# Performance work log

Measured on AMD Instinct MI355X. Metric: run time of the kernel, lower is better.

The kernel has to match this reference:

```python
import jax, jax.numpy as jnp
import numpy as np

WS = 8        # window_size
NH = 8        # num_heads
LN_EPS = 1e-5

# static relative-position index table [WS*WS, WS*WS], values in [0, (2*WS-1)**2)
def _rel_index(ws):
    coords = np.arange(ws)
    grid = np.stack(np.meshgrid(coords, coords, indexing='ij')).reshape(2, -1)  # [2, W2]
    rel = grid[:, :, None] - grid[:, None, :]            # [2, W2, W2]
    rel = rel.transpose(1, 2, 0).copy()                   # [W2, W2, 2]
    rel[..., 0] += ws - 1
    rel[..., 1] += ws - 1
    rel[..., 0] *= 2 * ws - 1
    return rel.sum(-1)                                    # [W2, W2]

REL_IDX = jnp.asarray(_rel_index(WS))


def _ln(x):
    # LayerNorm without affine params (elementwise_affine=False)
    mu = jnp.mean(x, axis=-1, keepdims=True)
    var = jnp.var(x, axis=-1, keepdims=True)
    return (x - mu) * jax.lax.rsqrt(var + LN_EPS)


def setup_inputs() -> dict:
    key = jax.random.key(0)
    ks = jax.random.split(key, 16)
    B, Hg, Wg, C = 8, 64, 64, 256
    L = Hg * Wg
    s = 0.02
    inp = {
        'x': jax.random.normal(ks[0], (B, L, C), jnp.float32),
        't_embed': jax.random.normal(ks[1], (B, C), jnp.float32),
        'H': Hg,
        'W': Wg,
        'adaln1_w': s * jax.random.normal(ks[2], (C, 2 * C), jnp.float32),
        'adaln1_b': jnp.zeros((2 * C,), jnp.float32),
        'adaln2_w': s * jax.random.normal(ks[3], (C, 2 * C), jnp.float32),
        'adaln2_b': jnp.zeros((2 * C,), jnp.float32),
        'bias_table': s * jax.random.normal(ks[4], ((2 * WS - 1) ** 2, NH), jnp.float32),
        'q_w': s * jax.random.normal(ks[5], (C, C), jnp.float32),
        'q_b': jnp.zeros((C,), jnp.float32),
        'k_w': s * jax.random.normal(ks[6], (C, C), jnp.float32),
        'k_b': jnp.zeros((C,), jnp.float32),
        'v_w': s * jax.random.normal(ks[7], (C, C), jnp.float32),
        'v_b': jnp.zeros((C,), jnp.float32),
        'o_w': s * jax.random.normal(ks[8], (C, C), jnp.float32),
        'o_b': jnp.zeros((C,), jnp.float32),
        'ffn1_w': s * jax.random.normal(ks[9], (C, 4 * C), jnp.float32),
        'ffn1_b': jnp.zeros((4 * C,), jnp.float32),
        'ffn2_w': s * jax.random.normal(ks[10], (4 * C, C), jnp.float32),
        'ffn2_b': jnp.zeros((C,), jnp.float32),
    }
    return inp


def reference(x, t_embed, H, W, adaln1_w, adaln1_b, adaln2_w, adaln2_b,
              bias_table, q_w, q_b, k_w, k_b, v_w, v_b, o_w, o_b,
              ffn1_w, ffn1_b, ffn2_w, ffn2_b):
    B, L, C = x.shape
    d = C // NH
    W2 = WS * WS
    sh = WS // 2  # cyclic shift (shifted=True)

    # --- AdaLN1 ---
    ss = t_embed @ adaln1_w + adaln1_b              # [B, 2C]
    scale, shift = jnp.split(ss, 2, axis=-1)
    xn = _ln(x) * (1.0 + scale[:, None, :]) + shift[:, None, :]

    # --- shifted window partition ---
    xg = xn.reshape(B, H, W, C)
    xg = jnp.roll(xg, (-sh, -sh), axis=(1, 2))
    xw = xg.reshape(B, H // WS, WS, W // WS, WS, C).transpose(0, 1, 3, 2, 4, 5)
    xw = xw.reshape(-1, W2, C)                       # [nwB, W2, C]
    nwB = xw.shape[0]

    # --- window attention with relative position bias ---
    q = (xw @ q_w + q_b).reshape(nwB, W2, NH, d).transpose(0, 2, 1, 3)
    k = (xw @ k_w + k_b).reshape(nwB, W2, NH, d).transpose(0, 2, 1, 3)
    v = (xw @ v_w + v_b).reshape(nwB, W2, NH, d).transpose(0, 2, 1, 3)
    logits = jnp.einsum('whqd,whkd->whqk', q, k) * (d ** -0.5)
    bias = bias_table[REL_IDX.reshape(-1)].reshape(W2, W2, NH).transpose(2, 0, 1)
    logits = logits + bias[None].astype(logits.dtype)
    attn = jax.nn.softmax(logits, axis=-1)
    out = jnp.einsum('whqk,whkd->whqd', attn, v).transpose(0, 2, 1, 3).reshape(nwB, W2, C)
    out = out @ o_w + o_b

    # --- window reverse + unshift ---
    xm = out.reshape(B, H // WS, W // WS, WS, WS, C).transpose(0, 1, 3, 2, 4, 5)
    xm = xm.reshape(B, H, W, C)
    xm = jnp.roll(xm, (sh, sh), axis=(1, 2))
    x = x + xm.reshape(B, L, C)

    # --- AdaLN2 + FFN (GELU exact, matching torch nn.GELU) ---
    ss2 = t_embed @ adaln2_w + adaln2_b
    sc2, sh2 = jnp.split(ss2, 2, axis=-1)
    xn2 = _ln(x) * (1.0 + sc2[:, None, :]) + sh2[:, None, :]
    h = jax.nn.gelu(xn2 @ ffn1_w + ffn1_b, approximate=False)
    x = x + (h @ ffn2_w + ffn2_b)
    return x
```

## Files before the change

kernel.cpp:

```cpp
#include <hip/hip_runtime.h>
#include <math.h>

#define WS_ 8
#define NH_ 8
#define C_ 256
#define B_ 8
#define M_ 32768
#define SH_ 4
#define LN_EPS 1e-5f
#define SL_ 8388608

typedef __attribute__((ext_vector_type(8))) short bf16x8;
typedef __attribute__((ext_vector_type(4))) float f32x4;

__device__ inline float b2f(unsigned short u) {
    union { unsigned int i; float f; } c; c.i = ((unsigned int)u) << 16; return c.f;
}
__device__ inline unsigned short f2b(float f) {
    union { unsigned int i; float f; } c; c.f = f;
    unsigned int u = c.i;
    return (unsigned short)((u + 0x7FFFu + ((u >> 16) & 1u)) >> 16);
}
__device__ inline float gelu_f(float x) {
    float t = 1.59576912160573f * (x + 0.044715f * x * x * x);
    return x / (1.f + __expf(-t));
}

__global__ void prep_k(const float* __restrict__ qw, const float* __restrict__ kw,
                       const float* __restrict__ vw, const float* __restrict__ ow,
                       const float* __restrict__ f1w, const float* __restrict__ f2w,
                       const float* __restrict__ qb, const float* __restrict__ kb,
                       const float* __restrict__ vb, const float* __restrict__ bt,
                       const float* __restrict__ te,
                       const float* __restrict__ a1w, const float* __restrict__ a1b,
                       const float* __restrict__ a2w, const float* __restrict__ a2b,
                       unsigned short* __restrict__ qkvT, unsigned short* __restrict__ oT,
                       unsigned short* __restrict__ f1T, unsigned short* __restrict__ f2T,
                       float* __restrict__ qkvB, float* __restrict__ bias_full,
                       float* __restrict__ ss1, float* __restrict__ ss2) {
    int t = blockIdx.x * 256 + threadIdx.x;
    if (t < 196608) {
        int n = t >> 8, k = t & 255;
        const float* w = n < 256 ? qw : (n < 512 ? kw : vw);
        qkvT[t] = f2b(w[k * 256 + (n & 255)]);
    } else if (t < 262144) {
        int i = t - 196608; int n = i >> 8, k = i & 255;
        oT[i] = f2b(ow[k * 256 + n]);
    } else if (t < 524288) {
        int i = t - 262144; int n = i >> 8, k = i & 255;
        f1T[i] = f2b(f1w[k * 1024 + n]);
    } else if (t < 786432) {
        int i = t - 524288; int n = i >> 10, k = i & 1023;
        f2T[i] = f2b(f2w[k * 256 + n]);
    } else if (t < 787200) {
        int i = t - 786432;
        qkvB[i] = i < 256 ? qb[i] : (i < 512 ? kb[i - 256] : vb[i - 512]);
    } else if (t < 819968) {
        int i = t - 787200;
        int head = i >> 12, qk = i & 4095;
        int q = qk >> 6, k = qk & 63;
        int qh = q >> 3, qw2 = q & 7, kh = k >> 3, kw2 = k & 7;
        bias_full[i] = bt[((qh - kh + 7) * 15 + (qw2 - kw2 + 7)) * 8 + head];
    } else if (t < 828160) {
        int i = t - 819968;
        int which = i >> 12;
        int rem = i & 4095;
        int b = rem >> 9, col = rem & 511;
        const float* w = which ? a2w : a1w;
        const float* bb = which ? a2b : a1b;
        const float* tr = te + b * C_;
        float acc = bb[col];
        for (int k = 0; k < C_; ++k) acc += tr[k] * w[k * 512 + col];
        (which ? ss2 : ss1)[b * 512 + col] = acc;
    }
}

__global__ __launch_bounds__(256) void ln_win_k(const float* __restrict__ x,
                                                const float* __restrict__ ss,
                                                unsigned short* __restrict__ xw) {
    int t = blockIdx.x * 4 + (threadIdx.x >> 6);
    int lane = threadIdx.x & 63;
    int b = t >> 12, rem = t & 4095;
    int hg = rem >> 6, wg = rem & 63;
    int hs = (hg + SH_) & 63, wsrc = (wg + SH_) & 63;
    size_t src = ((size_t)b << 12) + (hs << 6) + wsrc;
    float4 v = *(const float4*)&x[src * C_ + lane * 4];
    float s = v.x + v.y + v.z + v.w;
    float s2 = v.x * v.x + v.y * v.y + v.z * v.z + v.w * v.w;
#pragma unroll
    for (int m = 1; m < 64; m <<= 1) { s += __shfl_xor(s, m); s2 += __shfl_xor(s2, m); }
    float mu = s * (1.f / 256.f);
    float rstd = rsqrtf(s2 * (1.f / 256.f) - mu * mu + LN_EPS);
    float4 sc = *(const float4*)&ss[b * 512 + lane * 4];
    float4 sh = *(const float4*)&ss[b * 512 + 256 + lane * 4];
    int win = (b << 6) + ((hg >> 3) << 3) + (wg >> 3);
    int pos = ((hg & 7) << 3) + (wg & 7);
    ushort4 pk;
    pk.x = f2b((v.x - mu) * rstd * (1.f + sc.x) + sh.x);
    pk.y = f2b((v.y - mu) * rstd * (1.f + sc.y) + sh.y);
    pk.z = f2b((v.z - mu) * rstd * (1.f + sc.z) + sh.z);
    pk.w = f2b((v.w - mu) * rstd * (1.f + sc.w) + sh.w);
    *(ushort4*)(xw + (size_t)(win * 64 + pos) * C_ + lane * 4) = pk;
}

template <int KDIM, int MODE, int NT>
__global__ __launch_bounds__(512, 2) void gemmv_k(
    const unsigned short* __restrict__ A, const unsigned short* __restrict__ Bt,
    const float* __restrict__ bias, const float* __restrict__ res,
    void* __restrict__ Cout, const float* __restrict__ ss2,
    unsigned short* __restrict__ xn2out, int Nout) {
    constexpr int NCH = KDIM / 256;
    constexpr int NBUF = (NCH > 1) ? 2 : 1;
    __shared__ __align__(16) unsigned short As[NBUF][128 * 256];

    const int blk = blockIdx.x;
    const int xcd = blk & 7;
    const int idx = blk >> 3;
    const int mt = xcd + ((idx / NT) << 3);
    const int nt = idx % NT;
    const int bm = mt * 128, bn = nt * 256;
    const int tid = threadIdx.x;
    const int w = tid >> 6, lane = tid & 63;
    const int quad = lane >> 4, l16 = lane & 15;
    const int wrow = (w >> 2) * 64;
    const int wcol = (w & 3) * 64;
    const int srow16 = tid >> 5;
    const int sc = tid & 31;

    f32x4 acc[4][4] = {};

    auto stageA = [&](int buf, int kc) {
#pragma unroll
        for (int p = 0; p < 8; ++p) {
            int row = p * 16 + srow16;
            int g = sc ^ (row & 7);
            const unsigned short* ga = A + (size_t)(bm + row) * KDIM + kc * 256 + g * 8;
            unsigned short* la = &As[buf][row * 256 + sc * 8];
            __builtin_amdgcn_global_load_lds(
                (const __attribute__((address_space(1))) void*)ga,
                (__attribute__((address_space(3))) void*)la, 16, 0, 0);
        }
    };

    auto computeC = [&](int buf, int kc) {
        const unsigned short* bp = Bt + (size_t)(bn + wcol + l16) * KDIM + kc * 256 + quad * 8;
#pragma unroll
        for (int k8 = 0; k8 < 8; ++k8) {
            bf16x8 bfr[4], af[4];
#pragma unroll
            for (int j = 0; j < 4; ++j)
                bfr[j] = *(const bf16x8*)(bp + (size_t)j * 16 * KDIM + k8 * 32);
#pragma unroll
            for (int i = 0; i < 4; ++i) {
                int row = wrow + i * 16 + l16;
                int cidx = (k8 * 4 + quad) ^ (row & 7);
                af[i] = *(const bf16x8*)&As[buf][row * 256 + cidx * 8];
            }
            __builtin_amdgcn_s_setprio(1);
#pragma unroll
            for (int i = 0; i < 4; ++i)
#pragma unroll
                for (int j = 0; j < 4; ++j)
                    acc[i][j] = __builtin_amdgcn_mfma_f32_16x16x32_bf16(
                        bfr[j], af[i], acc[i][j], 0, 0, 0);
            __builtin_amdgcn_s_setprio(0);
        }
    };

    stageA(0, 0);
    asm volatile("s_waitcnt vmcnt(0)" ::: "memory");
    __builtin_amdgcn_s_barrier();
    if constexpr (NCH == 1) {
        computeC(0, 0);
    } else {
#pragma unroll
        for (int c = 0; c < NCH; ++c) {
            if (c + 1 < NCH) stageA((c + 1) & 1, c + 1);
            computeC(c & 1, c);
            if (c + 1 < NCH) {
                asm volatile("s_waitcnt vmcnt(0)" ::: "memory");
                __builtin_amdgcn_s_barrier();
            }
        }
    }

    if (MODE == 1) {
        float ps[4], ps2[4];
#pragma unroll
        for (int i = 0; i < 4; ++i) {
            const int row = bm + wrow + i * 16 + l16;
            int win = row >> 6, pos = row & 63;
            int b = win >> 6, wh = (win >> 3) & 7, ww = win & 7;
            int hg = (wh << 3) + (pos >> 3), wg = (ww << 3) + (pos & 7);
            int hd = (hg + SH_) & 63, wd = (wg + SH_) & 63;
            size_t rowbase = (((size_t)b << 12) + (hd << 6) + wd) * C_;
            float s = 0.f, s2 = 0.f;
#pragma unroll
            for (int j = 0; j < 4; ++j) {
                const int col = bn + wcol + j * 16 + quad * 4;
                float4 bv = *(const float4*)&bias[col];
                float4 rv = *(const float4*)&res[rowbase + col];
                float4 ov = {acc[i][j][0] + bv.x + rv.x, acc[i][j][1] + bv.y + rv.y,
                             acc[i][j][2] + bv.z + rv.z, acc[i][j][3] + bv.w + rv.w};
                *(float4*)&((float*)Cout)[rowbase + col] = ov;
                acc[i][j][0] = ov.x; acc[i][j][1] = ov.y;
                acc[i][j][2] = ov.z; acc[i][j][3] = ov.w;
                s += ov.x + ov.y + ov.z + ov.w;
                s2 += ov.x * ov.x + ov.y * ov.y + ov.z * ov.z + ov.w * ov.w;
            }
            ps[i] = s; ps2[i] = s2;
        }
#pragma unroll
        for (int i = 0; i < 4; ++i) {
            ps[i] += __shfl_xor(ps[i], 16);  ps[i] += __shfl_xor(ps[i], 32);
            ps2[i] += __shfl_xor(ps2[i], 16); ps2[i] += __shfl_xor(ps2[i], 32);
        }
        float* sred = (float*)&As[0][0];
        asm volatile("s_waitcnt lgkmcnt(0)" ::: "memory");
        __builtin_amdgcn_s_barrier();
        if (quad == 0) {
#pragma unroll
            for (int i = 0; i < 4; ++i) {
                int r = i * 16 + l16;
                sred[(w * 64 + r) * 2 + 0] = ps[i];
                sred[(w * 64 + r) * 2 + 1] = ps2[i];
            }
        }
        __builtin_amdgcn_s_barrier();
#pragma unroll
        for (int i = 0; i < 4; ++i) {
            int r = i * 16 + l16;
            float s = 0.f, s2 = 0.f;
#pragma unroll
            for (int cw = 0; cw < 4; ++cw) {
                s  += sred[(((w >> 2) * 4 + cw) * 64 + r) * 2 + 0];
                s2 += sred[(((w >> 2) * 4 + cw) * 64 + r) * 2 + 1];
            }
            float mu = s * (1.f / 256.f);
            float rstd = rsqrtf(s2 * (1.f / 256.f) - mu * mu + LN_EPS);
            const int row = bm + wrow + i * 16 + l16;
            int win = row >> 6, pos = row & 63;
            int b = win >> 6, wh = (win >> 3) & 7, ww = win & 7;
            int hg = (wh << 3) + (pos >> 3), wg = (ww << 3) + (pos & 7);
            int hd = (hg + SH_) & 63, wd = (wg + SH_) & 63;
            size_t rowbase = (((size_t)b << 12) + (hd << 6) + wd) * C_;
#pragma unroll
            for (int j = 0; j < 4; ++j) {
                const int col = bn + wcol + j * 16 + quad * 4;
                float4 scv = *(const float4*)&ss2[b * 512 + col];
                float4 shv = *(const float4*)&ss2[b * 512 + 256 + col];
                ushort4 pk;
                pk.x = f2b((acc[i][j][0] - mu) * rstd * (1.f + scv.x) + shv.x);
                pk.y = f2b((acc[i][j][1] - mu) * rstd * (1.f + scv.y) + shv.y);
                pk.z = f2b((acc[i][j][2] - mu) * rstd * (1.f + scv.z) + shv.z);
                pk.w = f2b((acc[i][j][3] - mu) * rstd * (1.f + scv.w) + shv.w);
                *(ushort4*)(xn2out + rowbase + col) = pk;
            }
        }
        return;
    }

#pragma unroll
    for (int i = 0; i < 4; ++i) {
        const int row = bm + wrow + i * 16 + l16;
        size_t rowbase = 0;
        if (MODE == 0) {
            int win = row >> 6, pos = row & 63;
            rowbase = (size_t)win * 16384 + pos * 32;
        } else {
            rowbase = (size_t)row * Nout;
        }
#pragma unroll
        for (int j = 0; j < 4; ++j) {
            const int col = bn + wcol + j * 16 + quad * 4;
            float4 bv = *(const float4*)&bias[col];
            float v0 = acc[i][j][0] + bv.x, v1 = acc[i][j][1] + bv.y;
            float v2 = acc[i][j][2] + bv.z, v3 = acc[i][j][3] + bv.w;
            if (MODE == 0) {
                int which = col >> 8, head = (col >> 5) & 7, dc = col & 31;
                ushort4 pk = {f2b(v0), f2b(v1), f2b(v2), f2b(v3)};
                *(ushort4*)((unsigned short*)Cout + (size_t)which * SL_ + rowbase +
                            head * 2048 + dc) = pk;
            } else if (MODE == 2) {
                ushort4 pk = {f2b(gelu_f(v0)), f2b(gelu_f(v1)),
                              f2b(gelu_f(v2)), f2b(gelu_f(v3))};
                *(ushort4*)((unsigned short*)Cout + rowbase + col) = pk;
            } else {
                float4 rv = *(const float4*)&res[rowbase + col];
                float4 ov = {v0 + rv.x, v1 + rv.y, v2 + rv.z, v3 + rv.w};
                *(float4*)&((float*)Cout)[rowbase + col] = ov;
            }
        }
    }
}

__global__ __launch_bounds__(256) void attn_mfma_k(
    const unsigned short* __restrict__ qkv, const float* __restrict__ bias_full,
    unsigned short* __restrict__ attn_out) {
    __shared__ __align__(16) unsigned short Pb[4][64 * 66];
    __shared__ __align__(16) unsigned short Vt[4][32 * 66];
    const int w = threadIdx.x >> 6, lane = threadIdx.x & 63;
    const int wh = blockIdx.x * 4 + w;
    const int win = wh >> 3, head = wh & 7;
    const int quad = lane >> 4, l16 = lane & 15;

    const unsigned short* qp = qkv + (size_t)win * 16384 + head * 2048;
    const unsigned short* kp = qp + SL_;
    const unsigned short* vp = qp + 2 * (size_t)SL_;

    {
        const uint4* v4 = (const uint4*)(vp + lane * 32);
        unsigned short* dst = &Vt[w][0];
#pragma unroll
        for (int c = 0; c < 4; ++c) {
            uint4 u = v4[c];
            unsigned int uu[4] = {u.x, u.y, u.z, u.w};
#pragma unroll
            for (int p = 0; p < 4; ++p) {
                int d0 = c * 8 + p * 2;
                dst[d0 * 66 + lane] = (unsigned short)(uu[p] & 0xffff);
                dst[(d0 + 1) * 66 + lane] = (unsigned short)(uu[p] >> 16);
            }
        }
    }

    bf16x8 qf[4], kf[4];
#pragma unroll
    for (int i = 0; i < 4; ++i) {
        qf[i] = *(const bf16x8*)(qp + (i * 16 + l16) * 32 + quad * 8);
        kf[i] = *(const bf16x8*)(kp + (i * 16 + l16) * 32 + quad * 8);
    }

    f32x4 s[4][4] = {};
#pragma unroll
    for (int i = 0; i < 4; ++i)
#pragma unroll
        for (int j = 0; j < 4; ++j)
            s[i][j] = __builtin_amdgcn_mfma_f32_16x16x32_bf16(qf[i], kf[j], s[i][j], 0, 0, 0);

    const float scale = 0.17677669529663687f;
    const float* bf = bias_full + head * 4096;
    float rs[4][4];
#pragma unroll
    for (int i = 0; i < 4; ++i) {
#pragma unroll
        for (int r = 0; r < 4; ++r) {
            int row = i * 16 + quad * 4 + r;
            float acc = 0.f;
#pragma unroll
            for (int j = 0; j < 4; ++j) {
                float e = __expf(s[i][j][r] * scale + bf[row * 64 + j * 16 + l16]);
                s[i][j][r] = e;
                acc += e;
            }
#pragma unroll
            for (int msk = 1; msk < 16; msk <<= 1) acc += __shfl_xor(acc, msk);
            rs[i][r] = 1.f / acc;
        }
    }

#pragma unroll
    for (int i = 0; i < 4; ++i)
#pragma unroll
        for (int j = 0; j < 4; ++j)
#pragma unroll
            for (int r = 0; r < 4; ++r)
                Pb[w][(i * 16 + quad * 4 + r) * 66 + j * 16 + l16] = f2b(s[i][j][r]);

    __syncthreads();

    f32x4 o[4][2] = {};
#pragma unroll
    for (int st = 0; st < 2; ++st) {
        bf16x8 bv[2];
#pragma unroll
        for (int jo = 0; jo < 2; ++jo)
            bv[jo] = *(const bf16x8*)&Vt[w][(jo * 16 + l16) * 66 + st * 32 + quad * 8];
#pragma unroll
        for (int i = 0; i < 4; ++i) {
            bf16x8 af = *(const bf16x8*)&Pb[w][(i * 16 + l16) * 66 + st * 32 + quad * 8];
#pragma unroll
            for (int jo = 0; jo < 2; ++jo)
                o[i][jo] = __builtin_amdgcn_mfma_f32_16x16x32_bf16(af, bv[jo], o[i][jo], 0, 0, 0);
        }
    }

#pragma unroll
    for (int i = 0; i < 4; ++i)
#pragma unroll
        for (int jo = 0; jo < 2; ++jo)
#pragma unroll
            for (int r = 0; r < 4; ++r) {
                int row = i * 16 + quad * 4 + r;
                int d = jo * 16 + l16;
                attn_out[((size_t)(win * 64 + row)) * C_ + head * 32 + d] =
                    f2b(o[i][jo][r] * rs[i][r]);
            }
}

extern "C" void kernel_launch(void* const* d_in, const int* in_sizes, int n_in,
                              void* d_out, int out_size, void* d_ws, size_t ws_size,
                              hipStream_t stream) {
    const float* x        = (const float*)d_in[0];
    const float* t_embed  = (const float*)d_in[1];
    const float* adaln1_w = (const float*)d_in[4];
    const float* adaln1_b = (const float*)d_in[5];
    const float* adaln2_w = (const float*)d_in[6];
    const float* adaln2_b = (const float*)d_in[7];
    const float* bt       = (const float*)d_in[8];
    const float* q_w = (const float*)d_in[9],  *q_b = (const float*)d_in[10];
    const float* k_w = (const float*)d_in[11], *k_b = (const float*)d_in[12];
    const float* v_w = (const float*)d_in[13], *v_b = (const float*)d_in[14];
    const float* o_w = (const float*)d_in[15], *o_b = (const float*)d_in[16];
    const float* f1_w = (const float*)d_in[17], *f1_b = (const float*)d_in[18];
    const float* f2_w = (const float*)d_in[19], *f2_b = (const float*)d_in[20];
    float* out = (float*)d_out;

    char* wsb = (char*)d_ws;
    float* ss1            = (float*)(wsb + 0);
    float* ss2            = (float*)(wsb + 16384);
    float* qkvB           = (float*)(wsb + 32768);
    unsigned short* qkvT  = (unsigned short*)(wsb + 36864);
    unsigned short* oT    = (unsigned short*)(wsb + 430080);
    unsigned short* f1T   = (unsigned short*)(wsb + 561152);
    unsigned short* f2T   = (unsigned short*)(wsb + 1085440);
    float* bias_full      = (float*)(wsb + 1609728);
    unsigned short* xw    = (unsigned short*)(wsb + 2097152);
    unsigned short* qkv   = (unsigned short*)(wsb + 18874368);
    unsigned short* attn  = (unsigned short*)(wsb + 69206016);
    unsigned short* xn2   = xw;
    unsigned short* hbuf  = qkv;
    float* x1             = (float*)(wsb + 85983232);

    prep_k<<<3235, 256, 0, stream>>>(q_w, k_w, v_w, o_w, f1_w, f2_w, q_b, k_b, v_b, bt,
                                     t_embed, adaln1_w, adaln1_b, adaln2_w, adaln2_b,
                                     qkvT, oT, f1T, f2T, qkvB, bias_full, ss1, ss2);
    ln_win_k<<<8192, 256, 0, stream>>>(x, ss1, xw);

    gemmv_k<256, 0, 3><<<768, 512, 0, stream>>>(xw, qkvT, qkvB, nullptr, qkv,
                                                nullptr, nullptr, 768);

    attn_mfma_k<<<1024, 256, 0, stream>>>(qkv, bias_full, attn);

    gemmv_k<256, 1, 1><<<256, 512, 0, stream>>>(attn, oT, o_b, x, x1,
                                                ss2, xn2, 256);
    gemmv_k<256, 2, 4><<<1024, 512, 0, stream>>>(xn2, f1T, f1_b, nullptr, hbuf,
                                                 nullptr, nullptr, 1024);
    gemmv_k<1024, 3, 1><<<256, 512, 0, stream>>>(hbuf, f2T, f2_b, x1, out,
                                                 nullptr, nullptr, 256);
}
```

Before: 317.4 us.

## Stage both GEMM operands through swizzled LDS with 128x128 tiles and K-chunking

Replaces the GEMM kernel that held a full 128x256 A tile in LDS and streamed B directly from global memory. The new kernel stages both A and B through XOR-swizzled LDS in 128-wide K chunks, using 128x128 output tiles and 256-thread blocks. The O-projection plus LayerNorm epilogue is split into its own kernel with the same LDS staging for A and B. The aim is to cut redundant global B reads and raise block count and occupancy. The cost is that loads and compute are no longer double-buffered, and each K chunk adds a barrier.

```diff
diff --git a/kernel.cpp b/kernel.cpp
--- a/kernel.cpp
+++ b/kernel.cpp
@@ -103,166 +103,70 @@
     *(ushort4*)(xw + (size_t)(win * 64 + pos) * C_ + lane * 4) = pk;
 }
 
-template <int KDIM, int MODE, int NT>
-__global__ __launch_bounds__(512, 2) void gemmv_k(
+template <int KDIM, int MODE, int NT, int MINW>
+__global__ __launch_bounds__(256, MINW) void gemm_bf16_k(
     const unsigned short* __restrict__ A, const unsigned short* __restrict__ Bt,
     const float* __restrict__ bias, const float* __restrict__ res,
-    void* __restrict__ Cout, const float* __restrict__ ss2,
-    unsigned short* __restrict__ xn2out, int Nout) {
-    constexpr int NCH = KDIM / 256;
-    constexpr int NBUF = (NCH > 1) ? 2 : 1;
-    __shared__ __align__(16) unsigned short As[NBUF][128 * 256];
-
+    void* __restrict__ Cout, int Nout) {
+    __shared__ __align__(16) unsigned short As[4][128 * 32];
+    __shared__ __align__(16) unsigned short Bs[4][128 * 32];
     const int blk = blockIdx.x;
     const int xcd = blk & 7;
     const int idx = blk >> 3;
     const int mt = xcd + ((idx / NT) << 3);
     const int nt = idx % NT;
-    const int bm = mt * 128, bn = nt * 256;
+    const int bm = mt * 128, bn = nt * 128;
     const int tid = threadIdx.x;
     const int w = tid >> 6, lane = tid & 63;
     const int quad = lane >> 4, l16 = lane & 15;
-    const int wrow = (w >> 2) * 64;
-    const int wcol = (w & 3) * 64;
-    const int srow16 = tid >> 5;
-    const int sc = tid & 31;
+    const int wm = (w >> 1) * 64, wn = (w & 1) * 64;
+    const int srow = lane >> 2;
+    const int qlog = ((lane & 3) ^ ((lane >> 3) & 3)) << 3;
+    const int rsw = ((l16 >> 1) & 3) << 3;
 
     f32x4 acc[4][4] = {};
 
-    auto stageA = [&](int buf, int kc) {
-#pragma unroll
-        for (int p = 0; p < 8; ++p) {
-            int row = p * 16 + srow16;
-            int g = sc ^ (row & 7);
-            const unsigned short* ga = A + (size_t)(bm + row) * KDIM + kc * 256 + g * 8;
-            unsigned short* la = &As[buf][row * 256 + sc * 8];
-            __builtin_amdgcn_global_load_lds(
-                (const __attribute__((address_space(1))) void*)ga,
-                (__attribute__((address_space(3))) void*)la, 16, 0, 0);
-        }
-    };
-
-    auto computeC = [&](int buf, int kc) {
-        const unsigned short* bp = Bt + (size_t)(bn + wcol + l16) * KDIM + kc * 256 + quad * 8;
-#pragma unroll
-        for (int k8 = 0; k8 < 8; ++k8) {
-            bf16x8 bfr[4], af[4];
+    for (int k0 = 0; k0 < KDIM; k0 += 128) {
+        if (k0) __syncthreads();
+#pragma unroll
+        for (int h = 0; h < 4; ++h) {
+#pragma unroll
+            for (int j = 0; j < 2; ++j) {
+                int r = j * 64 + w * 16 + srow;
+                const unsigned short* ga = A + (size_t)(bm + r) * KDIM + k0 + h * 32 + qlog;
+                unsigned short* la = &As[h][j * 2048 + w * 512 + lane * 8];
+                __builtin_amdgcn_global_load_lds(
+                    (const __attribute__((address_space(1))) void*)ga,
+                    (__attribute__((address_space(3))) void*)la, 16, 0, 0);
+                const unsigned short* gb = Bt + (size_t)(bn + r) * KDIM + k0 + h * 32 + qlog;
+                unsigned short* lb = &Bs[h][j * 2048 + w * 512 + lane * 8];
+                __builtin_amdgcn_global_load_lds(
+                    (const __attribute__((address_space(1))) void*)gb,
+                    (__attribute__((address_space(3))) void*)lb, 16, 0, 0);
+            }
+        }
+        __syncthreads();
+#pragma unroll
+        for (int h = 0; h < 4; ++h) {
+            bf16x8 af[4], bfr[4];
+#pragma unroll
+            for (int i = 0; i < 4; ++i)
+                af[i] = *(const bf16x8*)&As[h][(wm + i * 16 + l16) * 32 + ((quad << 3) ^ rsw)];
 #pragma unroll
             for (int j = 0; j < 4; ++j)
-                bfr[j] = *(const bf16x8*)(bp + (size_t)j * 16 * KDIM + k8 * 32);
-#pragma unroll
-            for (int i = 0; i < 4; ++i) {
-                int row = wrow + i * 16 + l16;
-                int cidx = (k8 * 4 + quad) ^ (row & 7);
-                af[i] = *(const bf16x8*)&As[buf][row * 256 + cidx * 8];
-            }
-            __builtin_amdgcn_s_setprio(1);
+                bfr[j] = *(const bf16x8*)&Bs[h][(wn + j * 16 + l16) * 32 + ((quad << 3) ^ rsw)];
 #pragma unroll
             for (int i = 0; i < 4; ++i)
 #pragma unroll
                 for (int j = 0; j < 4; ++j)
                     acc[i][j] = __builtin_amdgcn_mfma_f32_16x16x32_bf16(
                         bfr[j], af[i], acc[i][j], 0, 0, 0);
-            __builtin_amdgcn_s_setprio(0);
-        }
-    };
-
-    stageA(0, 0);
-    asm volatile("s_waitcnt vmcnt(0)" ::: "memory");
-    __builtin_amdgcn_s_barrier();
-    if constexpr (NCH == 1) {
-        computeC(0, 0);
-    } else {
-#pragma unroll
-        for (int c = 0; c < NCH; ++c) {
-            if (c + 1 < NCH) stageA((c + 1) & 1, c + 1);
-            computeC(c & 1, c);
-            if (c + 1 < NCH) {
-                asm volatile("s_waitcnt vmcnt(0)" ::: "memory");
-                __builtin_amdgcn_s_barrier();
-            }
-        }
-    }
-
-    if (MODE == 1) {
-        float ps[4], ps2[4];
-#pragma unroll
-        for (int i = 0; i < 4; ++i) {
-            const int row = bm + wrow + i * 16 + l16;
-            int win = row >> 6, pos = row & 63;
-            int b = win >> 6, wh = (win >> 3) & 7, ww = win & 7;
-            int hg = (wh << 3) + (pos >> 3), wg = (ww << 3) + (pos & 7);
-            int hd = (hg + SH_) & 63, wd = (wg + SH_) & 63;
-            size_t rowbase = (((size_t)b << 12) + (hd << 6) + wd) * C_;
-            float s = 0.f, s2 = 0.f;
-#pragma unroll
-            for (int j = 0; j < 4; ++j) {
-                const int col = bn + wcol + j * 16 + quad * 4;
-                float4 bv = *(const float4*)&bias[col];
-                float4 rv = *(const float4*)&res[rowbase + col];
-                float4 ov = {acc[i][j][0] + bv.x + rv.x, acc[i][j][1] + bv.y + rv.y,
-                             acc[i][j][2] + bv.z + rv.z, acc[i][j][3] + bv.w + rv.w};
-                *(float4*)&((float*)Cout)[rowbase + col] = ov;
-                acc[i][j][0] = ov.x; acc[i][j][1] = ov.y;
-                acc[i][j][2] = ov.z; acc[i][j][3] = ov.w;
-                s += ov.x + ov.y + ov.z + ov.w;
-                s2 += ov.x * ov.x + ov.y * ov.y + ov.z * ov.z + ov.w * ov.w;
-            }
-            ps[i] = s; ps2[i] = s2;
-        }
-#pragma unroll
-        for (int i = 0; i < 4; ++i) {
-            ps[i] += __shfl_xor(ps[i], 16);  ps[i] += __shfl_xor(ps[i], 32);
-            ps2[i] += __shfl_xor(ps2[i], 16); ps2[i] += __shfl_xor(ps2[i], 32);
-        }
-        float* sred = (float*)&As[0][0];
-        asm volatile("s_waitcnt lgkmcnt(0)" ::: "memory");
-        __builtin_amdgcn_s_barrier();
-        if (quad == 0) {
-#pragma unroll
-            for (int i = 0; i < 4; ++i) {
-                int r = i * 16 + l16;
-                sred[(w * 64 + r) * 2 + 0] = ps[i];
-                sred[(w * 64 + r) * 2 + 1] = ps2[i];
-            }
-        }
-        __builtin_amdgcn_s_barrier();
-#pragma unroll
-        for (int i = 0; i < 4; ++i) {
-            int r = i * 16 + l16;
-            float s = 0.f, s2 = 0.f;
-#pragma unroll
-            for (int cw = 0; cw < 4; ++cw) {
-                s  += sred[(((w >> 2) * 4 + cw) * 64 + r) * 2 + 0];
-                s2 += sred[(((w >> 2) * 4 + cw) * 64 + r) * 2 + 1];
-            }
-            float mu = s * (1.f / 256.f);
-            float rstd = rsqrtf(s2 * (1.f / 256.f) - mu * mu + LN_EPS);
-            const int row = bm + wrow + i * 16 + l16;
-            int win = row >> 6, pos = row & 63;
-            int b = win >> 6, wh = (win >> 3) & 7, ww = win & 7;
-            int hg = (wh << 3) + (pos >> 3), wg = (ww << 3) + (pos & 7);
-            int hd = (hg + SH_) & 63, wd = (wg + SH_) & 63;
-            size_t rowbase = (((size_t)b << 12) + (hd << 6) + wd) * C_;
-#pragma unroll
-            for (int j = 0; j < 4; ++j) {
-                const int col = bn + wcol + j * 16 + quad * 4;
-                float4 scv = *(const float4*)&ss2[b * 512 + col];
-                float4 shv = *(const float4*)&ss2[b * 512 + 256 + col];
-                ushort4 pk;
-                pk.x = f2b((acc[i][j][0] - mu) * rstd * (1.f + scv.x) + shv.x);
-                pk.y = f2b((acc[i][j][1] - mu) * rstd * (1.f + scv.y) + shv.y);
-                pk.z = f2b((acc[i][j][2] - mu) * rstd * (1.f + scv.z) + shv.z);
-                pk.w = f2b((acc[i][j][3] - mu) * rstd * (1.f + scv.w) + shv.w);
-                *(ushort4*)(xn2out + rowbase + col) = pk;
-            }
-        }
-        return;
-    }
-
-#pragma unroll
-    for (int i = 0; i < 4; ++i) {
-        const int row = bm + wrow + i * 16 + l16;
+        }
+    }
+
+#pragma unroll
+    for (int i = 0; i < 4; ++i) {
+        const int row = bm + wm + i * 16 + l16;
         size_t rowbase = 0;
         if (MODE == 0) {
             int win = row >> 6, pos = row & 63;
@@ -272,7 +176,7 @@
         }
 #pragma unroll
         for (int j = 0; j < 4; ++j) {
-            const int col = bn + wcol + j * 16 + quad * 4;
+            const int col = bn + wn + j * 16 + quad * 4;
             float4 bv = *(const float4*)&bias[col];
             float v0 = acc[i][j][0] + bv.x, v1 = acc[i][j][1] + bv.y;
             float v2 = acc[i][j][2] + bv.z, v3 = acc[i][j][3] + bv.w;
@@ -290,6 +194,132 @@
                 float4 ov = {v0 + rv.x, v1 + rv.y, v2 + rv.z, v3 + rv.w};
                 *(float4*)&((float*)Cout)[rowbase + col] = ov;
             }
+        }
+    }
+}
+
+__global__ __launch_bounds__(512, 2) void oproj_ln_k(
+    const unsigned short* __restrict__ A, const unsigned short* __restrict__ Bt,
+    const float* __restrict__ bias, const float* __restrict__ res,
+    float* __restrict__ x1, const float* __restrict__ ss2,
+    unsigned short* __restrict__ xn2) {
+    __shared__ __align__(16) unsigned short As[4][128 * 32];
+    __shared__ __align__(16) unsigned short Bs[4][256 * 32];
+    const int bm = blockIdx.x * 128;
+    const int tid = threadIdx.x;
+    const int w = tid >> 6, lane = tid & 63;
+    const int quad = lane >> 4, l16 = lane & 15;
+    const int wrow = (w >> 2) * 64, wcol = (w & 3) * 64;
+    const int rsw = ((l16 >> 1) & 3) << 3;
+    const int srow = tid >> 2;
+    const int gch = ((tid & 3) ^ ((srow >> 1) & 3)) << 3;
+
+    f32x4 acc[4][4] = {};
+
+    for (int k0 = 0; k0 < 256; k0 += 128) {
+        if (k0) __syncthreads();
+#pragma unroll
+        for (int h = 0; h < 4; ++h) {
+            const unsigned short* ga = A + (size_t)(bm + srow) * 256 + k0 + h * 32 + gch;
+            __builtin_amdgcn_global_load_lds(
+                (const __attribute__((address_space(1))) void*)ga,
+                (__attribute__((address_space(3))) void*)&As[h][tid * 8], 16, 0, 0);
+#pragma unroll
+            for (int s = 0; s < 2; ++s) {
+                const unsigned short* gb = Bt + (size_t)(s * 128 + srow) * 256 + k0 + h * 32 + gch;
+                __builtin_amdgcn_global_load_lds(
+                    (const __attribute__((address_space(1))) void*)gb,
+                    (__attribute__((address_space(3))) void*)&Bs[h][s * 4096 + tid * 8], 16, 0, 0);
+            }
+        }
+        __syncthreads();
+#pragma unroll
+        for (int h = 0; h < 4; ++h) {
+            bf16x8 af[4], bfr[4];
+#pragma unroll
+            for (int i = 0; i < 4; ++i)
+                af[i] = *(const bf16x8*)&As[h][(wrow + i * 16 + l16) * 32 + ((quad << 3) ^ rsw)];
+#pragma unroll
+            for (int j = 0; j < 4; ++j)
+                bfr[j] = *(const bf16x8*)&Bs[h][(wcol + j * 16 + l16) * 32 + ((quad << 3) ^ rsw)];
+#pragma unroll
+            for (int i = 0; i < 4; ++i)
+#pragma unroll
+                for (int j = 0; j < 4; ++j)
+                    acc[i][j] = __builtin_amdgcn_mfma_f32_16x16x32_bf16(
+                        bfr[j], af[i], acc[i][j], 0, 0, 0);
+        }
+    }
+
+    float ps[4], ps2[4];
+#pragma unroll
+    for (int i = 0; i < 4; ++i) {
+        const int row = bm + wrow + i * 16 + l16;
+        int win = row >> 6, pos = row & 63;
+        int b = win >> 6, wh = (win >> 3) & 7, ww = win & 7;
+        int hg = (wh << 3) + (pos >> 3), wg = (ww << 3) + (pos & 7);
+        int hd = (hg + SH_) & 63, wd = (wg + SH_) & 63;
+        size_t rowbase = (((size_t)b << 12) + (hd << 6) + wd) * C_;
+        float s = 0.f, s2 = 0.f;
+#pragma unroll
+        for (int j = 0; j < 4; ++j) {
+            const int col = wcol + j * 16 + quad * 4;
+            float4 bv = *(const float4*)&bias[col];
+            float4 rv = *(const float4*)&res[rowbase + col];
+            float4 ov = {acc[i][j][0] + bv.x + rv.x, acc[i][j][1] + bv.y + rv.y,
+                         acc[i][j][2] + bv.z + rv.z, acc[i][j][3] + bv.w + rv.w};
+            *(float4*)&x1[rowbase + col] = ov;
+            acc[i][j][0] = ov.x; acc[i][j][1] = ov.y;
+            acc[i][j][2] = ov.z; acc[i][j][3] = ov.w;
+            s += ov.x + ov.y + ov.z + ov.w;
+            s2 += ov.x * ov.x + ov.y * ov.y + ov.z * ov.z + ov.w * ov.w;
+        }
+        ps[i] = s; ps2[i] = s2;
+    }
+#pragma unroll
+    for (int i = 0; i < 4; ++i) {
+        ps[i] += __shfl_xor(ps[i], 16);  ps[i] += __shfl_xor(ps[i], 32);
+        ps2[i] += __shfl_xor(ps2[i], 16); ps2[i] += __shfl_xor(ps2[i], 32);
+    }
+    float* sred = (float*)&As[0][0];
+    __syncthreads();
+    if (quad == 0) {
+#pragma unroll
+        for (int i = 0; i < 4; ++i) {
+            int r = i * 16 + l16;
+            sred[(w * 64 + r) * 2 + 0] = ps[i];
+            sred[(w * 64 + r) * 2 + 1] = ps2[i];
+        }
+    }
+    __syncthreads();
+#pragma unroll
+    for (int i = 0; i < 4; ++i) {
+        int r = i * 16 + l16;
+        float s = 0.f, s2 = 0.f;
+#pragma unroll
+        for (int cw = 0; cw < 4; ++cw) {
+            s  += sred[(((w >> 2) * 4 + cw) * 64 + r) * 2 + 0];
+            s2 += sred[(((w >> 2) * 4 + cw) * 64 + r) * 2 + 1];
+        }
+        float mu = s * (1.f / 256.f);
+        float rstd = rsqrtf(s2 * (1.f / 256.f) - mu * mu + LN_EPS);
+        const int row = bm + wrow + i * 16 + l16;
+        int win = row >> 6, pos = row & 63;
+        int b = win >> 6, wh = (win >> 3) & 7, ww = win & 7;
+        int hg = (wh << 3) + (pos >> 3), wg = (ww << 3) + (pos & 7);
+        int hd = (hg + SH_) & 63, wd = (wg + SH_) & 63;
+        size_t rowbase = (((size_t)b << 12) + (hd << 6) + wd) * C_;
+#pragma unroll
+        for (int j = 0; j < 4; ++j) {
+            const int col = wcol + j * 16 + quad * 4;
+            float4 scv = *(const float4*)&ss2[b * 512 + col];
+            float4 shv = *(const float4*)&ss2[b * 512 + 256 + col];
+            ushort4 pk;
+            pk.x = f2b((acc[i][j][0] - mu) * rstd * (1.f + scv.x) + shv.x);
+            pk.y = f2b((acc[i][j][1] - mu) * rstd * (1.f + scv.y) + shv.y);
+            pk.z = f2b((acc[i][j][2] - mu) * rstd * (1.f + scv.z) + shv.z);
+            pk.w = f2b((acc[i][j][3] - mu) * rstd * (1.f + scv.w) + shv.w);
+            *(ushort4*)(xn2 + rowbase + col) = pk;
         }
     }
 }
@@ -437,15 +467,12 @@
                                      qkvT, oT, f1T, f2T, qkvB, bias_full, ss1, ss2);
     ln_win_k<<<8192, 256, 0, stream>>>(x, ss1, xw);
 
-    gemmv_k<256, 0, 3><<<768, 512, 0, stream>>>(xw, qkvT, qkvB, nullptr, qkv,
-                                                nullptr, nullptr, 768);
+    gemm_bf16_k<256, 0, 6, 2><<<1536, 256, 0, stream>>>(xw, qkvT, qkvB, nullptr, qkv, 768);
 
     attn_mfma_k<<<1024, 256, 0, stream>>>(qkv, bias_full, attn);
 
-    gemmv_k<256, 1, 1><<<256, 512, 0, stream>>>(attn, oT, o_b, x, x1,
-                                                ss2, xn2, 256);
-    gemmv_k<256, 2, 4><<<1024, 512, 0, stream>>>(xn2, f1T, f1_b, nullptr, hbuf,
-                                                 nullptr, nullptr, 1024);
-    gemmv_k<1024, 3, 1><<<256, 512, 0, stream>>>(hbuf, f2T, f2_b, x1, out,
-                                                 nullptr, nullptr, 256);
-}
+    oproj_ln_k<<<256, 512, 0, stream>>>(attn, oT, o_b, x, x1, ss2, xn2);
+
+    gemm_bf16_k<256, 2, 8, 2><<<2048, 256, 0, stream>>>(xn2, f1T, f1_b, nullptr, hbuf, 1024);
+    gemm_bf16_k<1024, 3, 2, 2><<<512, 256, 0, stream>>>(hbuf, f2T, f2_b, x1, out, 256);
+}
```

Result: faster. 270.8 us (-14.7%).
